# Performance work log

Measured on AMD Instinct MI355X. Metric: run time of the kernel, lower is better.

## Reference

```python
import math
import jax, jax.numpy as jnp
import numpy as np

L = 16
LOG2T = 19
T = 1 << LOG2T
FDIM = 2
N_MIN = 16
N_MAX = 512
N_PTS = 1 << 20
B_GROWTH = math.exp((math.log(N_MAX) - math.log(N_MIN)) / (L - 1))
RESOLUTIONS = [math.floor(N_MIN * (B_GROWTH ** i)) for i in range(L)]
BB_MIN = jnp.zeros((3,), jnp.float32)
BB_MAX = jnp.ones((3,), jnp.float32)
VERTICES = jnp.array([[0,0,0],[0,0,1],[0,1,0],[0,1,1],[1,0,0],[1,0,1],[1,1,0],[1,1,1]], dtype=jnp.uint32)
PRIMES = jnp.array([1, 2654435761, 805459861], dtype=jnp.uint32)
HASH_MASK = jnp.uint32((1 << 19) - 1)


def setup_inputs() -> dict:
    key = jax.random.key(0)
    k1, k2 = jax.random.split(key)
    xyz = jax.random.uniform(k1, (N_PTS, 3), dtype=jnp.float32)  # inside unit bb
    tables = jax.random.uniform(k2, (L, T, FDIM), dtype=jnp.float32,
                                minval=-1e-4, maxval=1e-4)
    return {"xyz": xyz, "tables": tables}


def _level(xyz, table, res):
    cell = (BB_MAX - BB_MIN) / res                                  # [3]
    min_index = jnp.floor((xyz - BB_MIN) / cell).astype(jnp.int32)  # [N,3]
    min_v = min_index.astype(jnp.float32) * cell + BB_MIN           # [N,3]
    max_v = min_v + cell
    # 8 corner indices, hash with spatial primes (wrap-around multiply == low-bit equal)
    idx = min_index[:, None, :].astype(jnp.uint32) + VERTICES       # [N,8,3]
    hp = idx * PRIMES                                               # uint32 wrap
    h = ((hp[..., 0] ^ hp[..., 1] ^ hp[..., 2]) & HASH_MASK).astype(jnp.int32)  # [N,8]
    emb = table[h]                                                  # [N,8,F] gather
    # trilinear interpolation
    d = (xyz - min_v) / (max_v - min_v)                             # [N,3]
    dx, dy, dz = d[:, 0:1], d[:, 1:2], d[:, 2:3]
    c00 = emb[:, 0] * (1 - dx) + emb[:, 4] * dx
    c01 = emb[:, 1] * (1 - dx) + emb[:, 5] * dx
    c10 = emb[:, 2] * (1 - dx) + emb[:, 6] * dx
    c11 = emb[:, 3] * (1 - dx) + emb[:, 7] * dx
    c0 = c00 * (1 - dy) + c10 * dy
    c1 = c01 * (1 - dy) + c11 * dy
    return c0 * (1 - dz) + c1 * dz                                  # [N,F]


def reference(xyz, tables):
    outs = [_level(xyz, tables[i], RESOLUTIONS[i]) for i in range(L)]
    return jnp.concatenate(outs, axis=-1)                           # [N, L*F]
```

## Files before the change

kernel.cpp:

```cpp
#include <hip/hip_runtime.h>
#include <math.h>
#include <stdint.h>

#define NLEVELS 16
#define TSIZE   (1u << 19)
#define HMASK   (TSIZE - 1u)
#define P1 2654435761u
#define P2 805459861u

typedef float v2f __attribute__((ext_vector_type(2)));
typedef float v4f __attribute__((ext_vector_type(4)));

struct LevelParams {
    float    cell[NLEVELS];
    uint32_t slvl[8][3];
    uint32_t scnt[8][3];
    uint32_t sbase[8][3];
};

__device__ __forceinline__ uint32_t bf16_rne(float f) {
    uint32_t b = __float_as_uint(f);
    return (b + 0x7FFFu + ((b >> 16) & 1u)) >> 16;
}

__global__ __launch_bounds__(256) void convert_tables_kernel(
    const v2f* __restrict__ tables, uint32_t* __restrict__ tab16,
    unsigned int nEntries)
{
    unsigned int i = blockIdx.x * 256u + threadIdx.x;
    if (i >= nEntries) return;
    v2f v = __builtin_nontemporal_load(&tables[i]);
    tab16[i] = (bf16_rne(v.x) << 16) | bf16_rne(v.y);
}

__global__ __launch_bounds__(256) void hashgrid_compute_kernel(
    const float* __restrict__ xyz,
    const uint32_t* __restrict__ tab16,
    v2f* __restrict__ stage,
    LevelParams lp,
    unsigned int npts)
{
    unsigned int b   = blockIdx.x;
    unsigned int xcd = b & 7u;
    unsigned int j   = b >> 3;

    unsigned int level, chunk;
    if (j & 1u) {
        unsigned int t = j >> 1;
        unsigned int s = 0;
        while (s < 2u && t >= lp.scnt[xcd][s]) { t -= lp.scnt[xcd][s]; ++s; }
        level = lp.slvl[xcd][s];
        chunk = lp.sbase[xcd][s] + t;
    } else {
        level = 8u + xcd;
        chunk = j >> 1;
    }
    unsigned int n = chunk * 256u + threadIdx.x;

    float x = xyz[n * 3 + 0];
    float y = xyz[n * 3 + 1];
    float z = xyz[n * 3 + 2];

    float cell = lp.cell[level];

    float fx = floorf(x / cell);
    float fy = floorf(y / cell);
    float fz = floorf(z / cell);

    float mvx = fx * cell, mvy = fy * cell, mvz = fz * cell;
    float dnx = (mvx + cell) - mvx;
    float dny = (mvy + cell) - mvy;
    float dnz = (mvz + cell) - mvz;

    float dx = (x - mvx) * __builtin_amdgcn_rcpf(dnx);
    float dy = (y - mvy) * __builtin_amdgcn_rcpf(dny);
    float dz = (z - mvz) * __builtin_amdgcn_rcpf(dnz);

    unsigned int ix = (unsigned int)(int)fx;
    unsigned int iy = (unsigned int)(int)fy;
    unsigned int iz = (unsigned int)(int)fz;

    unsigned int hx0 = ix,      hx1 = ix + 1u;
    unsigned int hy0 = iy * P1, hy1 = hy0 + P1;
    unsigned int hz0 = iz * P2, hz1 = hz0 + P2;

    const uint32_t* __restrict__ tab = tab16 + (size_t)level * TSIZE;

    uint32_t u0 = tab[(hx0 ^ hy0 ^ hz0) & HMASK];
    uint32_t u1 = tab[(hx0 ^ hy0 ^ hz1) & HMASK];
    uint32_t u2 = tab[(hx0 ^ hy1 ^ hz0) & HMASK];
    uint32_t u3 = tab[(hx0 ^ hy1 ^ hz1) & HMASK];
    uint32_t u4 = tab[(hx1 ^ hy0 ^ hz0) & HMASK];
    uint32_t u5 = tab[(hx1 ^ hy0 ^ hz1) & HMASK];
    uint32_t u6 = tab[(hx1 ^ hy1 ^ hz0) & HMASK];
    uint32_t u7 = tab[(hx1 ^ hy1 ^ hz1) & HMASK];

    #define UX(u) __uint_as_float((u) & 0xFFFF0000u)
    #define UY(u) __uint_as_float((u) << 16)

    float wx0 = 1.0f - dx, wy0 = 1.0f - dy, wz0 = 1.0f - dz;

    float c00x = UX(u0) * wx0 + UX(u4) * dx;
    float c00y = UY(u0) * wx0 + UY(u4) * dx;
    float c01x = UX(u1) * wx0 + UX(u5) * dx;
    float c01y = UY(u1) * wx0 + UY(u5) * dx;
    float c10x = UX(u2) * wx0 + UX(u6) * dx;
    float c10y = UY(u2) * wx0 + UY(u6) * dx;
    float c11x = UX(u3) * wx0 + UX(u7) * dx;
    float c11y = UY(u3) * wx0 + UY(u7) * dx;

    #undef UX
    #undef UY

    float c0x = c00x * wy0 + c10x * dy;
    float c0y = c00y * wy0 + c10y * dy;
    float c1x = c01x * wy0 + c11x * dy;
    float c1y = c01y * wy0 + c11y * dy;

    v2f r;
    r.x = c0x * wz0 + c1x * dz;
    r.y = c0y * wz0 + c1y * dz;

    __builtin_nontemporal_store(r, &stage[(size_t)level * npts + n]);
}

__global__ __launch_bounds__(256) void transpose_kernel(
    const v2f* __restrict__ stage, v4f* __restrict__ out4, unsigned int npts)
{
    __shared__ v2f lds[256][17];
    unsigned int tid  = threadIdx.x;
    unsigned int base = blockIdx.x * 256u;

#pragma unroll
    for (int l = 0; l < NLEVELS; ++l)
        lds[tid][l] = __builtin_nontemporal_load(&stage[(size_t)l * npts + base + tid]);

    __syncthreads();

#pragma unroll
    for (int it = 0; it < 8; ++it) {
        unsigned int i = it * 256u + tid;
        unsigned int p = i >> 3;
        unsigned int k = i & 7u;
        v2f a = lds[p][2 * k];
        v2f c = lds[p][2 * k + 1];
        v4f w; w.x = a.x; w.y = a.y; w.z = c.x; w.w = c.y;
        __builtin_nontemporal_store(w, &out4[(size_t)blockIdx.x * 2048u + i]);
    }
}

__global__ __launch_bounds__(256) void hashgrid_direct_kernel(
    const float* __restrict__ xyz,
    const float* __restrict__ tables,
    float2* __restrict__ out,
    LevelParams lp,
    unsigned int total)
{
    unsigned int t = blockIdx.x * 256u + threadIdx.x;
    if (t >= total) return;
    unsigned int n = t >> 4;
    unsigned int l = t & 15u;

    float x = xyz[n * 3 + 0], y = xyz[n * 3 + 1], z = xyz[n * 3 + 2];
    float cell = lp.cell[l];
    float fx = floorf(x / cell), fy = floorf(y / cell), fz = floorf(z / cell);
    float mvx = fx * cell, mvy = fy * cell, mvz = fz * cell;
    float dnx = (mvx + cell) - mvx, dny = (mvy + cell) - mvy, dnz = (mvz + cell) - mvz;
    float dx = (x - mvx) * __builtin_amdgcn_rcpf(dnx);
    float dy = (y - mvy) * __builtin_amdgcn_rcpf(dny);
    float dz = (z - mvz) * __builtin_amdgcn_rcpf(dnz);
    unsigned int ix = (unsigned int)(int)fx, iy = (unsigned int)(int)fy, iz = (unsigned int)(int)fz;
    unsigned int hx0 = ix, hx1 = ix + 1u;
    unsigned int hy0 = iy * P1, hy1 = hy0 + P1;
    unsigned int hz0 = iz * P2, hz1 = hz0 + P2;
    const float2* __restrict__ tab = (const float2*)tables + (size_t)l * TSIZE;
    float2 e0 = tab[(hx0 ^ hy0 ^ hz0) & HMASK];
    float2 e1 = tab[(hx0 ^ hy0 ^ hz1) & HMASK];
    float2 e2 = tab[(hx0 ^ hy1 ^ hz0) & HMASK];
    float2 e3 = tab[(hx0 ^ hy1 ^ hz1) & HMASK];
    float2 e4 = tab[(hx1 ^ hy0 ^ hz0) & HMASK];
    float2 e5 = tab[(hx1 ^ hy0 ^ hz1) & HMASK];
    float2 e6 = tab[(hx1 ^ hy1 ^ hz0) & HMASK];
    float2 e7 = tab[(hx1 ^ hy1 ^ hz1) & HMASK];
    float wx0 = 1.0f - dx, wy0 = 1.0f - dy, wz0 = 1.0f - dz;
    float c00x = e0.x * wx0 + e4.x * dx, c00y = e0.y * wx0 + e4.y * dx;
    float c01x = e1.x * wx0 + e5.x * dx, c01y = e1.y * wx0 + e5.y * dx;
    float c10x = e2.x * wx0 + e6.x * dx, c10y = e2.y * wx0 + e6.y * dx;
    float c11x = e3.x * wx0 + e7.x * dx, c11y = e3.y * wx0 + e7.y * dx;
    float c0x = c00x * wy0 + c10x * dy, c0y = c00y * wy0 + c10y * dy;
    float c1x = c01x * wy0 + c11x * dy, c1y = c01y * wy0 + c11y * dy;
    out[t] = make_float2(c0x * wz0 + c1x * dz, c0y * wz0 + c1y * dz);
}

extern "C" void kernel_launch(void* const* d_in, const int* in_sizes, int n_in,
                              void* d_out, int out_size, void* d_ws, size_t ws_size,
                              hipStream_t stream)
{
    const float* xyz    = (const float*)d_in[0];
    const float* tables = (const float*)d_in[1];

    LevelParams lp;
    double bg = exp((log(512.0) - log(16.0)) / 15.0);
    for (int i = 0; i < NLEVELS; ++i) {
        int res = (int)floor(16.0 * pow(bg, (double)i));
        lp.cell[i] = 1.0f / (float)res;
    }

    unsigned int npts = (unsigned int)(in_sizes[0] / 3);
    size_t tabBytes   = (size_t)NLEVELS * TSIZE * 4u;
    size_t stageBytes = (size_t)npts * NLEVELS * sizeof(v2f);

    if (ws_size >= tabBytes + stageBytes && (npts & 255u) == 0u) {
        uint32_t* tab16 = (uint32_t*)d_ws;
        v2f* stage = (v2f*)((char*)d_ws + tabBytes);

        unsigned int nEntries = NLEVELS * TSIZE;
        hipLaunchKernelGGL(convert_tables_kernel,
                           dim3((nEntries + 255u) / 256u), dim3(256), 0, stream,
                           (const v2f*)tables, tab16, nEntries);

        unsigned int chunks = npts / 256u;

        for (int x = 0; x < 8; ++x)
            for (int s = 0; s < 3; ++s) {
                lp.slvl[x][s] = 0; lp.scnt[x][s] = 0; lp.sbase[x][s] = 0;
            }
        if ((chunks & 3u) == 0u) {
            unsigned int q = chunks / 4u;
            for (int x = 0; x < 4; ++x) {
                lp.slvl[x][0] = 7;         lp.scnt[x][0] = q;      lp.sbase[x][0] = (unsigned)x * q;
                lp.slvl[x][1] = (unsigned)x; lp.scnt[x][1] = 3u * q; lp.sbase[x][1] = 0;
            }
            lp.slvl[4][0] = 6; lp.scnt[4][0] = 2u * q; lp.sbase[4][0] = 0;
            lp.slvl[4][1] = 0; lp.scnt[4][1] = q;      lp.sbase[4][1] = 3u * q;
            lp.slvl[4][2] = 1; lp.scnt[4][2] = q;      lp.sbase[4][2] = 3u * q;
            lp.slvl[5][0] = 6; lp.scnt[5][0] = 2u * q; lp.sbase[5][0] = 2u * q;
            lp.slvl[5][1] = 2; lp.scnt[5][1] = q;      lp.sbase[5][1] = 3u * q;
            lp.slvl[5][2] = 3; lp.scnt[5][2] = q;      lp.sbase[5][2] = 3u * q;
            lp.slvl[6][0] = 5; lp.scnt[6][0] = chunks; lp.sbase[6][0] = 0;
            lp.slvl[7][0] = 4; lp.scnt[7][0] = chunks; lp.sbase[7][0] = 0;
        } else {
            for (int x = 0; x < 8; ++x) {
                lp.slvl[x][0] = (unsigned)x; lp.scnt[x][0] = chunks; lp.sbase[x][0] = 0;
            }
        }

        hipLaunchKernelGGL(hashgrid_compute_kernel,
                           dim3(NLEVELS * chunks), dim3(256), 0, stream,
                           xyz, tab16, stage, lp, npts);

        hipLaunchKernelGGL(transpose_kernel,
                           dim3(chunks), dim3(256), 0, stream,
                           stage, (v4f*)d_out, npts);
    } else {
        unsigned int total = npts * (unsigned int)NLEVELS;
        hipLaunchKernelGGL(hashgrid_direct_kernel,
                           dim3((total + 255u) / 256u), dim3(256), 0, stream,
                           xyz, tables, (float2*)d_out, lp, total);
    }
}
```

Baseline: 544.4 us.

## Precompute per-cell packed corner embeddings for coarse levels to replace hash gathers

Adds a build kernel that, for the six or seven coarsest levels, materializes the 8 bf16-packed corner embeddings of every grid cell contiguously. The compute kernel then fetches a point's corners with two 16-byte vector loads instead of eight scattered hashed gathers, and only the finer levels still use the converted hash table. The XCD/level block schedule is rebalanced for the new split. In exchange it adds a precompute pass and a workspace region of about 16 MB. If the workspace is too small it falls back to the slow direct kernel.

```diff
diff --git a/kernel.cpp b/kernel.cpp
--- a/kernel.cpp
+++ b/kernel.cpp
@@ -10,12 +10,16 @@
 
 typedef float v2f __attribute__((ext_vector_type(2)));
 typedef float v4f __attribute__((ext_vector_type(4)));
+typedef uint32_t u32x4 __attribute__((ext_vector_type(4)));
 
 struct LevelParams {
     float    cell[NLEVELS];
-    uint32_t slvl[8][3];
-    uint32_t scnt[8][3];
-    uint32_t sbase[8][3];
+    uint32_t res[NLEVELS];
+    uint32_t cellOff[NLEVELS];
+    uint32_t HB;
+    uint32_t slvl[8][4];
+    uint32_t scnt[8][4];
+    uint32_t sbase[8][4];
 };
 
 __device__ __forceinline__ uint32_t bf16_rne(float f) {
@@ -24,18 +28,58 @@
 }
 
 __global__ __launch_bounds__(256) void convert_tables_kernel(
-    const v2f* __restrict__ tables, uint32_t* __restrict__ tab16,
+    const v2f* __restrict__ tablesOff,
+    uint32_t* __restrict__ tab16,
     unsigned int nEntries)
 {
     unsigned int i = blockIdx.x * 256u + threadIdx.x;
     if (i >= nEntries) return;
-    v2f v = __builtin_nontemporal_load(&tables[i]);
+    v2f v = __builtin_nontemporal_load(&tablesOff[i]);
     tab16[i] = (bf16_rne(v.x) << 16) | bf16_rne(v.y);
+}
+
+__global__ __launch_bounds__(256) void build_cells_kernel(
+    const float2* __restrict__ tables,
+    uint32_t* __restrict__ cells,
+    LevelParams lp, unsigned int totCells)
+{
+    unsigned int i = blockIdx.x * 256u + threadIdx.x;
+    if (i >= totCells) return;
+
+    unsigned int l = 0;
+#pragma unroll
+    for (unsigned int k = 1; k < 7u; ++k)
+        if (k < lp.HB && i >= lp.cellOff[k]) l = k;
+
+    unsigned int c   = i - lp.cellOff[l];
+    unsigned int res = lp.res[l];
+    unsigned int cz  = c % res;
+    unsigned int t   = c / res;
+    unsigned int cy  = t % res;
+    unsigned int cx  = t / res;
+
+    const float2* __restrict__ tab = tables + (size_t)l * TSIZE;
+    uint32_t u[8];
+#pragma unroll
+    for (int k = 0; k < 8; ++k) {
+        unsigned int vx = cx + (unsigned)(k >> 2);
+        unsigned int vy = cy + (unsigned)((k >> 1) & 1);
+        unsigned int vz = cz + (unsigned)(k & 1);
+        unsigned int h  = (vx ^ (vy * P1) ^ (vz * P2)) & HMASK;
+        float2 e = tab[h];
+        u[k] = (bf16_rne(e.x) << 16) | bf16_rne(e.y);
+    }
+    uint32_t* dst = cells + (size_t)i * 8u;
+    u32x4 q0; q0.x = u[0]; q0.y = u[1]; q0.z = u[2]; q0.w = u[3];
+    u32x4 q1; q1.x = u[4]; q1.y = u[5]; q1.z = u[6]; q1.w = u[7];
+    *(u32x4*)dst       = q0;
+    *(u32x4*)(dst + 4) = q1;
 }
 
 __global__ __launch_bounds__(256) void hashgrid_compute_kernel(
     const float* __restrict__ xyz,
     const uint32_t* __restrict__ tab16,
+    const uint32_t* __restrict__ cells,
     v2f* __restrict__ stage,
     LevelParams lp,
     unsigned int npts)
@@ -48,7 +92,7 @@
     if (j & 1u) {
         unsigned int t = j >> 1;
         unsigned int s = 0;
-        while (s < 2u && t >= lp.scnt[xcd][s]) { t -= lp.scnt[xcd][s]; ++s; }
+        while (s < 3u && t >= lp.scnt[xcd][s]) { t -= lp.scnt[xcd][s]; ++s; }
         level = lp.slvl[xcd][s];
         chunk = lp.sbase[xcd][s] + t;
     } else {
@@ -80,20 +124,34 @@
     unsigned int iy = (unsigned int)(int)fy;
     unsigned int iz = (unsigned int)(int)fz;
 
-    unsigned int hx0 = ix,      hx1 = ix + 1u;
-    unsigned int hy0 = iy * P1, hy1 = hy0 + P1;
-    unsigned int hz0 = iz * P2, hz1 = hz0 + P2;
-
-    const uint32_t* __restrict__ tab = tab16 + (size_t)level * TSIZE;
-
-    uint32_t u0 = tab[(hx0 ^ hy0 ^ hz0) & HMASK];
-    uint32_t u1 = tab[(hx0 ^ hy0 ^ hz1) & HMASK];
-    uint32_t u2 = tab[(hx0 ^ hy1 ^ hz0) & HMASK];
-    uint32_t u3 = tab[(hx0 ^ hy1 ^ hz1) & HMASK];
-    uint32_t u4 = tab[(hx1 ^ hy0 ^ hz0) & HMASK];
-    uint32_t u5 = tab[(hx1 ^ hy0 ^ hz1) & HMASK];
-    uint32_t u6 = tab[(hx1 ^ hy1 ^ hz0) & HMASK];
-    uint32_t u7 = tab[(hx1 ^ hy1 ^ hz1) & HMASK];
+    uint32_t u0, u1, u2, u3, u4, u5, u6, u7;
+
+    if (level < lp.HB) {
+        unsigned int res = lp.res[level];
+        unsigned int c = (ix * res + iy) * res + iz;
+        const u32x4* __restrict__ ct =
+            (const u32x4*)cells + 2u * ((size_t)lp.cellOff[level] + c);
+        u32x4 q0 = ct[0];
+        u32x4 q1 = ct[1];
+        u0 = q0.x; u1 = q0.y; u2 = q0.z; u3 = q0.w;
+        u4 = q1.x; u5 = q1.y; u6 = q1.z; u7 = q1.w;
+    } else {
+        unsigned int hx0 = ix,      hx1 = ix + 1u;
+        unsigned int hy0 = iy * P1, hy1 = hy0 + P1;
+        unsigned int hz0 = iz * P2, hz1 = hz0 + P2;
+
+        const uint32_t* __restrict__ tab =
+            tab16 + (size_t)(level - lp.HB) * TSIZE;
+
+        u0 = tab[(hx0 ^ hy0 ^ hz0) & HMASK];
+        u1 = tab[(hx0 ^ hy0 ^ hz1) & HMASK];
+        u2 = tab[(hx0 ^ hy1 ^ hz0) & HMASK];
+        u3 = tab[(hx0 ^ hy1 ^ hz1) & HMASK];
+        u4 = tab[(hx1 ^ hy0 ^ hz0) & HMASK];
+        u5 = tab[(hx1 ^ hy0 ^ hz1) & HMASK];
+        u6 = tab[(hx1 ^ hy1 ^ hz0) & HMASK];
+        u7 = tab[(hx1 ^ hy1 ^ hz1) & HMASK];
+    }
 
     #define UX(u) __uint_as_float((u) & 0xFFFF0000u)
     #define UY(u) __uint_as_float((u) << 16)
@@ -201,44 +259,87 @@
 
     LevelParams lp;
     double bg = exp((log(512.0) - log(16.0)) / 15.0);
+    unsigned int resv[NLEVELS];
     for (int i = 0; i < NLEVELS; ++i) {
         int res = (int)floor(16.0 * pow(bg, (double)i));
+        resv[i] = (unsigned int)res;
+        lp.res[i]  = (unsigned int)res;
         lp.cell[i] = 1.0f / (float)res;
     }
 
     unsigned int npts = (unsigned int)(in_sizes[0] / 3);
-    size_t tabBytes   = (size_t)NLEVELS * TSIZE * 4u;
     size_t stageBytes = (size_t)npts * NLEVELS * sizeof(v2f);
 
-    if (ws_size >= tabBytes + stageBytes && (npts & 255u) == 0u) {
+    unsigned int HB = 0;
+    size_t tabBytes = 0, cellsCnt = 0;
+    for (unsigned int tryHB = 7; tryHB >= 6; --tryHB) {
+        size_t cc = 0;
+        for (unsigned int l = 0; l < tryHB; ++l)
+            cc += (size_t)resv[l] * resv[l] * resv[l];
+        size_t tb = (size_t)(NLEVELS - tryHB) * TSIZE * 4u;
+        if (ws_size >= tb + cc * 32u + stageBytes && (npts & 255u) == 0u) {
+            HB = tryHB; tabBytes = tb; cellsCnt = cc; break;
+        }
+    }
+
+    if (HB >= 6u) {
+        lp.HB = HB;
+        size_t off = 0;
+        for (unsigned int l = 0; l < NLEVELS; ++l) {
+            lp.cellOff[l] = (l < HB) ? (uint32_t)off : 0u;
+            if (l < HB) off += (size_t)resv[l] * resv[l] * resv[l];
+        }
+
         uint32_t* tab16 = (uint32_t*)d_ws;
-        v2f* stage = (v2f*)((char*)d_ws + tabBytes);
-
-        unsigned int nEntries = NLEVELS * TSIZE;
+        uint32_t* cells = (uint32_t*)((char*)d_ws + tabBytes);
+        v2f* stage = (v2f*)((char*)d_ws + tabBytes + cellsCnt * 32u);
+
+        unsigned int nEntries = (NLEVELS - HB) * TSIZE;
         hipLaunchKernelGGL(convert_tables_kernel,
-                           dim3((nEntries + 255u) / 256u), dim3(256), 0, stream,
-                           (const v2f*)tables, tab16, nEntries);
+                           dim3(nEntries / 256u), dim3(256), 0, stream,
+                           (const v2f*)tables + (size_t)HB * TSIZE, tab16, nEntries);
+
+        unsigned int totCells = (unsigned int)cellsCnt;
+        hipLaunchKernelGGL(build_cells_kernel,
+                           dim3((totCells + 255u) / 256u), dim3(256), 0, stream,
+                           (const float2*)tables, cells, lp, totCells);
 
         unsigned int chunks = npts / 256u;
 
         for (int x = 0; x < 8; ++x)
-            for (int s = 0; s < 3; ++s) {
+            for (int s = 0; s < 4; ++s) {
                 lp.slvl[x][s] = 0; lp.scnt[x][s] = 0; lp.sbase[x][s] = 0;
             }
         if ((chunks & 3u) == 0u) {
             unsigned int q = chunks / 4u;
-            for (int x = 0; x < 4; ++x) {
-                lp.slvl[x][0] = 7;         lp.scnt[x][0] = q;      lp.sbase[x][0] = (unsigned)x * q;
-                lp.slvl[x][1] = (unsigned)x; lp.scnt[x][1] = 3u * q; lp.sbase[x][1] = 0;
+            if (HB == 6u) {
+                for (unsigned x = 0; x < 4; ++x) {
+                    lp.slvl[x][0] = 7; lp.scnt[x][0] = q; lp.sbase[x][0] = x * q;
+                    lp.slvl[x][1] = x; lp.scnt[x][1] = 3u * q; lp.sbase[x][1] = 0;
+                }
+                for (unsigned x = 4; x < 8; ++x) {
+                    lp.slvl[x][0] = 6; lp.scnt[x][0] = q; lp.sbase[x][0] = (x - 4u) * q;
+                }
+                lp.slvl[4][1] = 4; lp.scnt[4][1] = 3u * q; lp.sbase[4][1] = 0;
+                lp.slvl[5][1] = 5; lp.scnt[5][1] = 3u * q; lp.sbase[5][1] = 0;
+                lp.slvl[6][1] = 4; lp.scnt[6][1] = q; lp.sbase[6][1] = 3u * q;
+                lp.slvl[6][2] = 0; lp.scnt[6][2] = q; lp.sbase[6][2] = 3u * q;
+                lp.slvl[6][3] = 1; lp.scnt[6][3] = q; lp.sbase[6][3] = 3u * q;
+                lp.slvl[7][1] = 5; lp.scnt[7][1] = q; lp.sbase[7][1] = 3u * q;
+                lp.slvl[7][2] = 2; lp.scnt[7][2] = q; lp.sbase[7][2] = 3u * q;
+                lp.slvl[7][3] = 3; lp.scnt[7][3] = q; lp.sbase[7][3] = 3u * q;
+            } else {
+                for (unsigned x = 0; x < 4; ++x) {
+                    lp.slvl[x][0] = 7; lp.scnt[x][0] = q; lp.sbase[x][0] = x * q;
+                    lp.slvl[x][1] = x; lp.scnt[x][1] = 3u * q; lp.sbase[x][1] = 0;
+                }
+                lp.slvl[4][0] = 4; lp.scnt[4][0] = chunks; lp.sbase[4][0] = 0;
+                lp.slvl[5][0] = 5; lp.scnt[5][0] = chunks; lp.sbase[5][0] = 0;
+                lp.slvl[6][0] = 6; lp.scnt[6][0] = chunks; lp.sbase[6][0] = 0;
+                for (unsigned s = 0; s < 4; ++s) {
+                    lp.slvl[7][s] = s; lp.scnt[7][s] = q; lp.sbase[7][s] = 3u * q;
+                }
             }
-            lp.slvl[4][0] = 6; lp.scnt[4][0] = 2u * q; lp.sbase[4][0] = 0;
-            lp.slvl[4][1] = 0; lp.scnt[4][1] = q;      lp.sbase[4][1] = 3u * q;
-            lp.slvl[4][2] = 1; lp.scnt[4][2] = q;      lp.sbase[4][2] = 3u * q;
-            lp.slvl[5][0] = 6; lp.scnt[5][0] = 2u * q; lp.sbase[5][0] = 2u * q;
-            lp.slvl[5][1] = 2; lp.scnt[5][1] = q;      lp.sbase[5][1] = 3u * q;
-            lp.slvl[5][2] = 3; lp.scnt[5][2] = q;      lp.sbase[5][2] = 3u * q;
-            lp.slvl[6][0] = 5; lp.scnt[6][0] = chunks; lp.sbase[6][0] = 0;
-            lp.slvl[7][0] = 4; lp.scnt[7][0] = chunks; lp.sbase[7][0] = 0;
         } else {
             for (int x = 0; x < 8; ++x) {
                 lp.slvl[x][0] = (unsigned)x; lp.scnt[x][0] = chunks; lp.sbase[x][0] = 0;
@@ -247,10 +348,10 @@
 
         hipLaunchKernelGGL(hashgrid_compute_kernel,
                            dim3(NLEVELS * chunks), dim3(256), 0, stream,
-                           xyz, tab16, stage, lp, npts);
+                           xyz, tab16, cells, stage, lp, npts);
 
         hipLaunchKernelGGL(transpose_kernel,
-                           dim3(chunks), dim3(256), 0, stream,
+                           dim3(npts / 256u), dim3(256), 0, stream,
                            stage, (v4f*)d_out, npts);
     } else {
         unsigned int total = npts * (unsigned int)NLEVELS;
```

Result: slower. 672.5 us (+23.5%).

## Reorder block schedule: fine levels first, coarse levels after, rebalance per-XCD work

Applied to the files above, without the earlier changes.

The block-to-(level,chunk) mapping changes from interleaving fine and coarse levels to running all fine-level (8-15) blocks first and the coarse-level blocks afterwards. The coarse-level split across XCDs is also rebalanced: XCDs 6 and 7 now share levels 4 and 5 rather than each taking a whole level. The aim is to keep each XCD's L2 working set to one hash table at a time and to even out per-XCD work. xyz loads are made nontemporal, which may cost reuse since every point is read once per level.

```diff
diff --git a/kernel.cpp b/kernel.cpp
--- a/kernel.cpp
+++ b/kernel.cpp
@@ -13,9 +13,9 @@
 
 struct LevelParams {
     float    cell[NLEVELS];
-    uint32_t slvl[8][3];
-    uint32_t scnt[8][3];
-    uint32_t sbase[8][3];
+    uint32_t slvl[8][4];
+    uint32_t scnt[8][4];
+    uint32_t sbase[8][4];
 };
 
 __device__ __forceinline__ uint32_t bf16_rne(float f) {
@@ -38,28 +38,29 @@
     const uint32_t* __restrict__ tab16,
     v2f* __restrict__ stage,
     LevelParams lp,
-    unsigned int npts)
+    unsigned int npts,
+    unsigned int chunks)
 {
     unsigned int b   = blockIdx.x;
     unsigned int xcd = b & 7u;
     unsigned int j   = b >> 3;
 
     unsigned int level, chunk;
-    if (j & 1u) {
-        unsigned int t = j >> 1;
+    if (j >= chunks) {
+        unsigned int t = j - chunks;
         unsigned int s = 0;
-        while (s < 2u && t >= lp.scnt[xcd][s]) { t -= lp.scnt[xcd][s]; ++s; }
+        while (s < 3u && t >= lp.scnt[xcd][s]) { t -= lp.scnt[xcd][s]; ++s; }
         level = lp.slvl[xcd][s];
         chunk = lp.sbase[xcd][s] + t;
     } else {
         level = 8u + xcd;
-        chunk = j >> 1;
+        chunk = j;
     }
     unsigned int n = chunk * 256u + threadIdx.x;
 
-    float x = xyz[n * 3 + 0];
-    float y = xyz[n * 3 + 1];
-    float z = xyz[n * 3 + 2];
+    float x = __builtin_nontemporal_load(&xyz[n * 3 + 0]);
+    float y = __builtin_nontemporal_load(&xyz[n * 3 + 1]);
+    float z = __builtin_nontemporal_load(&xyz[n * 3 + 2]);
 
     float cell = lp.cell[level];
 
@@ -216,20 +217,20 @@
 
         unsigned int nEntries = NLEVELS * TSIZE;
         hipLaunchKernelGGL(convert_tables_kernel,
-                           dim3((nEntries + 255u) / 256u), dim3(256), 0, stream,
+                           dim3(nEntries / 256u), dim3(256), 0, stream,
                            (const v2f*)tables, tab16, nEntries);
 
         unsigned int chunks = npts / 256u;
 
         for (int x = 0; x < 8; ++x)
-            for (int s = 0; s < 3; ++s) {
+            for (int s = 0; s < 4; ++s) {
                 lp.slvl[x][s] = 0; lp.scnt[x][s] = 0; lp.sbase[x][s] = 0;
             }
         if ((chunks & 3u) == 0u) {
             unsigned int q = chunks / 4u;
-            for (int x = 0; x < 4; ++x) {
-                lp.slvl[x][0] = 7;         lp.scnt[x][0] = q;      lp.sbase[x][0] = (unsigned)x * q;
-                lp.slvl[x][1] = (unsigned)x; lp.scnt[x][1] = 3u * q; lp.sbase[x][1] = 0;
+            for (unsigned x = 0; x < 4; ++x) {
+                lp.slvl[x][0] = 7; lp.scnt[x][0] = q;      lp.sbase[x][0] = x * q;
+                lp.slvl[x][1] = x; lp.scnt[x][1] = 3u * q; lp.sbase[x][1] = 0;
             }
             lp.slvl[4][0] = 6; lp.scnt[4][0] = 2u * q; lp.sbase[4][0] = 0;
             lp.slvl[4][1] = 0; lp.scnt[4][1] = q;      lp.sbase[4][1] = 3u * q;
@@ -237,8 +238,10 @@
             lp.slvl[5][0] = 6; lp.scnt[5][0] = 2u * q; lp.sbase[5][0] = 2u * q;
             lp.slvl[5][1] = 2; lp.scnt[5][1] = q;      lp.sbase[5][1] = 3u * q;
             lp.slvl[5][2] = 3; lp.scnt[5][2] = q;      lp.sbase[5][2] = 3u * q;
-            lp.slvl[6][0] = 5; lp.scnt[6][0] = chunks; lp.sbase[6][0] = 0;
-            lp.slvl[7][0] = 4; lp.scnt[7][0] = chunks; lp.sbase[7][0] = 0;
+            lp.slvl[6][0] = 5; lp.scnt[6][0] = 3u * q; lp.sbase[6][0] = 0;
+            lp.slvl[6][1] = 4; lp.scnt[6][1] = q;      lp.sbase[6][1] = 3u * q;
+            lp.slvl[7][0] = 4; lp.scnt[7][0] = 3u * q; lp.sbase[7][0] = 0;
+            lp.slvl[7][1] = 5; lp.scnt[7][1] = q;      lp.sbase[7][1] = 3u * q;
         } else {
             for (int x = 0; x < 8; ++x) {
                 lp.slvl[x][0] = (unsigned)x; lp.scnt[x][0] = chunks; lp.sbase[x][0] = 0;
@@ -247,10 +250,10 @@
 
         hipLaunchKernelGGL(hashgrid_compute_kernel,
                            dim3(NLEVELS * chunks), dim3(256), 0, stream,
-                           xyz, tab16, stage, lp, npts);
+                           xyz, tab16, stage, lp, npts, chunks);
 
         hipLaunchKernelGGL(transpose_kernel,
-                           dim3(chunks), dim3(256), 0, stream,
+                           dim3(npts / 256u), dim3(256), 0, stream,
                            stage, (v4f*)d_out, npts);
     } else {
         unsigned int total = npts * (unsigned int)NLEVELS;
```

New measurement: 595.0 us. 9.3% more time.
